# Performance work log

Hardware: AMD Instinct MI355X
Metric: run time of the kernel (lower is better)

Reference implementation:

```python
import jax, jax.numpy as jnp
import numpy as np

N = 100000      # nodes
E = 1600000     # edges (avg degree 16)
D_IN = 256
D_OUT = 128

def setup_inputs() -> dict:
    key = jax.random.key(0)
    k1, k2, k3, k4, k5 = jax.random.split(key, 5)
    x = jax.random.normal(k1, (N, D_IN), dtype=jnp.float32)
    row = jax.random.randint(k2, (E,), 0, N)           # destination node of each edge (adj row index)
    col = jax.random.randint(k3, (E,), 0, N)           # source node (adj col index)
    vals = jnp.ones((E,), dtype=jnp.float32)           # adjacency values
    W = jax.random.normal(k4, (D_IN, D_OUT), dtype=jnp.float32) * (1.0 / np.sqrt(D_IN))
    b = jax.random.normal(k5, (D_OUT,), dtype=jnp.float32) * 0.01
    return {"x": x, "row": row, "col": col, "vals": vals, "W": W, "b": b}

def reference(x, row, col, vals, W, b):
    # support = Linear(x)
    support = x @ W + b                                   # [N, D_OUT]
    # symmetric normalization: D^-1/2 A D^-1/2 (degree = row sums of adj)
    deg = jax.ops.segment_sum(vals, row, num_segments=N)  # [N]
    d_inv_sqrt = jnp.where(deg > 0, jax.lax.rsqrt(jnp.maximum(deg, 1e-12)), 0.0)
    norm_vals = vals * d_inv_sqrt[row] * d_inv_sqrt[col]  # [E]
    # output = spmm(adj_norm, support): gather source features, scale, scatter-add to rows
    out = jax.ops.segment_sum(norm_vals[:, None] * support[col], row, num_segments=N)  # [N, D_OUT]
    return out
```

## Files before the change

kernel.cpp:

```cpp
#include <hip/hip_runtime.h>
#include <hip/hip_bf16.h>

#define DIN 256
#define DOUT 128

typedef float f32x4 __attribute__((ext_vector_type(4)));
typedef __bf16 bf16x8 __attribute__((ext_vector_type(8)));
typedef unsigned short u16x8 __attribute__((ext_vector_type(8)));

__device__ __forceinline__ unsigned short f2bf(float f) {
    __bf16 h = (__bf16)f;
    return *(unsigned short*)&h;
}

__global__ void gcn_zero(int* __restrict__ cnt, int N) {
    int i = blockIdx.x * blockDim.x + threadIdx.x;
    if (i < N) cnt[i] = 0;
}

__global__ void gcn_count(const int* __restrict__ row, int* __restrict__ cnt,
                          int* __restrict__ rank, int E) {
    int e = blockIdx.x * blockDim.x + threadIdx.x;
    if (e < E) {
        int r = row[e];
        rank[e] = atomicAdd(&cnt[r], 1);
    }
}

__global__ void gcn_scan_partial(const int* __restrict__ cnt, int* __restrict__ blk, int N) {
    int b = blockIdx.x, t = threadIdx.x;
    int base = b * 1024 + t * 4;
    int s = 0;
#pragma unroll
    for (int k = 0; k < 4; ++k) { int i = base + k; if (i < N) s += cnt[i]; }
    for (int d = 32; d >= 1; d >>= 1) s += __shfl_down(s, d, 64);
    __shared__ int wsum[4];
    int lane = t & 63, wid = t >> 6;
    if (lane == 0) wsum[wid] = s;
    __syncthreads();
    if (t == 0) blk[b] = wsum[0] + wsum[1] + wsum[2] + wsum[3];
}

__global__ void gcn_scan_blk(int* __restrict__ blk, int nblk) {
    if (threadIdx.x == 0) {
        int run = 0;
        for (int i = 0; i < nblk; ++i) { int v = blk[i]; blk[i] = run; run += v; }
    }
}

__global__ void gcn_scan_final(const int* __restrict__ cnt, const int* __restrict__ blk,
                               int* __restrict__ row_ptr, int N, int E) {
    int b = blockIdx.x, t = threadIdx.x;
    int base = b * 1024 + t * 4;
    int v[4]; int s = 0;
#pragma unroll
    for (int k = 0; k < 4; ++k) { int i = base + k; v[k] = (i < N) ? cnt[i] : 0; s += v[k]; }
    int mysum = s;
    int lane = t & 63, wid = t >> 6;
    for (int d = 1; d < 64; d <<= 1) {
        int tt = __shfl_up(s, d, 64);
        if (lane >= d) s += tt;
    }
    __shared__ int wsum[4];
    if (lane == 63) wsum[wid] = s;
    __syncthreads();
    int woff = 0;
    for (int w = 0; w < wid; ++w) woff += wsum[w];
    int excl = blk[b] + woff + (s - mysum);
#pragma unroll
    for (int k = 0; k < 4; ++k) {
        int i = base + k;
        if (i < N) row_ptr[i] = excl;
        excl += v[k];
    }
    if (b == (int)gridDim.x - 1 && t == (int)blockDim.x - 1) row_ptr[N] = E;
}

__global__ void gcn_fill(const int* __restrict__ row, const int* __restrict__ col,
                         const float* __restrict__ vals, const int* __restrict__ row_ptr,
                         const int* __restrict__ rank, int2* __restrict__ csr, int E) {
    int e = blockIdx.x * blockDim.x + threadIdx.x;
    if (e < E) {
        int r = row[e];
        int p = row_ptr[r] + rank[e];
        int2 pk;
        pk.x = col[e];
        pk.y = __float_as_int(vals[e]);
        csr[p] = pk;
    }
}

__global__ void gcn_degdinv(const int* __restrict__ row_ptr, const int2* __restrict__ csr,
                            float* __restrict__ dinv, int N) {
    int r = blockIdx.x * blockDim.x + threadIdx.x;
    if (r < N) {
        int b = row_ptr[r], e = row_ptr[r + 1];
        float s = 0.f;
        for (int j = b; j < e; ++j) s += __int_as_float(csr[j].y);
        dinv[r] = (s > 0.f) ? rsqrtf(fmaxf(s, 1e-12f)) : 0.f;
    }
}

__global__ void gcn_norm(const int* __restrict__ row_ptr, const float* __restrict__ dinv,
                         int2* __restrict__ csr, int N) {
    int r = blockIdx.x * blockDim.x + threadIdx.x;
    if (r < N) {
        int b = row_ptr[r], e = row_ptr[r + 1];
        float dr = dinv[r];
        for (int j = b; j < e; ++j) {
            int2 p = csr[j];
            csr[j].y = __float_as_int(__int_as_float(p.y) * dr * dinv[p.x]);
        }
    }
}

__global__ void gcn_wconv(const float* __restrict__ W, unsigned short* __restrict__ Wt) {
    int id = blockIdx.x * blockDim.x + threadIdx.x;
    int c = id >> 8;
    int k = id & 255;
    Wt[c * 256 + k] = f2bf(W[k * DOUT + c]);
}

__global__ __launch_bounds__(256) void gcn_gemm(const float* __restrict__ x,
                                                const unsigned short* __restrict__ Wt,
                                                const float* __restrict__ bias,
                                                unsigned short* __restrict__ support, int N) {
    __shared__ unsigned short xs[128][72];
    __shared__ unsigned short wl[128][72];

    int t = threadIdx.x;
    int n0 = blockIdx.x * 128;
    int l = t & 63;
    int w = t >> 6;
    int w32 = w * 32;
    int lr = l & 15;
    int lk = (l >> 4) * 8;

    f32x4 acc[2][8] = {};

    int srow = t >> 1;
    int skk = (t & 1) * 32;

    for (int kt = 0; kt < DIN; kt += 64) {
        {
            float4 f[8];
            if (n0 + srow < N) {
                const float4* src = (const float4*)&x[(size_t)(n0 + srow) * DIN + kt + skk];
#pragma unroll
                for (int i = 0; i < 8; ++i) f[i] = src[i];
            } else {
#pragma unroll
                for (int i = 0; i < 8; ++i) f[i] = make_float4(0, 0, 0, 0);
            }
#pragma unroll
            for (int i = 0; i < 4; ++i) {
                u16x8 pk;
                pk[0] = f2bf(f[2 * i].x);     pk[1] = f2bf(f[2 * i].y);
                pk[2] = f2bf(f[2 * i].z);     pk[3] = f2bf(f[2 * i].w);
                pk[4] = f2bf(f[2 * i + 1].x); pk[5] = f2bf(f[2 * i + 1].y);
                pk[6] = f2bf(f[2 * i + 1].z); pk[7] = f2bf(f[2 * i + 1].w);
                *(u16x8*)&xs[srow][skk + 8 * i] = pk;
            }
        }
        {
            const u16x8* src = (const u16x8*)&Wt[(size_t)srow * DIN + kt + skk];
#pragma unroll
            for (int i = 0; i < 4; ++i) *(u16x8*)&wl[srow][skk + 8 * i] = src[i];
        }
        __syncthreads();
#pragma unroll
        for (int ks = 0; ks < 2; ++ks) {
            bf16x8 a[2], b[8];
#pragma unroll
            for (int m = 0; m < 2; ++m)
                a[m] = *(const bf16x8*)&xs[w32 + m * 16 + lr][ks * 32 + lk];
#pragma unroll
            for (int n = 0; n < 8; ++n)
                b[n] = *(const bf16x8*)&wl[n * 16 + lr][ks * 32 + lk];
#pragma unroll
            for (int m = 0; m < 2; ++m)
#pragma unroll
                for (int n = 0; n < 8; ++n)
                    acc[m][n] = __builtin_amdgcn_mfma_f32_16x16x32_bf16(a[m], b[n], acc[m][n], 0, 0, 0);
        }
        __syncthreads();
    }

    float bias_v[8];
#pragma unroll
    for (int n = 0; n < 8; ++n) bias_v[n] = bias[n * 16 + lr];

    int rbase = n0 + w32 + (l >> 4) * 4;
#pragma unroll
    for (int m = 0; m < 2; ++m) {
#pragma unroll
        for (int r = 0; r < 4; ++r) {
            int rowi = rbase + m * 16 + r;
            if (rowi < N) {
                unsigned short* dst = &support[(size_t)rowi * DOUT + lr];
#pragma unroll
                for (int n = 0; n < 8; ++n)
                    dst[n * 16] = f2bf(acc[m][n][r] + bias_v[n]);
            }
        }
    }
}

__global__ __launch_bounds__(256) void gcn_spmm(const int* __restrict__ row_ptr,
                                                const int2* __restrict__ csr,
                                                const unsigned short* __restrict__ support,
                                                float* __restrict__ out, int N) {
    int wid = threadIdx.x >> 6;
    int lane = threadIdx.x & 63;
    int r = blockIdx.x * 4 + wid;
    if (r >= N) return;
    int beg = row_ptr[r], end = row_ptr[r + 1];
    float accx = 0.f, accy = 0.f;

    for (int base = beg; base < end; base += 64) {
        int nj = end - base; if (nj > 64) nj = 64;
        int2 e = make_int2(0, 0);
        if (base + lane < end) e = csr[base + lane];
        for (int j = 0; j < nj; ++j) {
            int c = __shfl(e.x, j, 64);
            float v = __int_as_float(__shfl(e.y, j, 64));
            unsigned int p = *(const unsigned int*)&support[(size_t)c * DOUT + lane * 2];
            accx += v * __uint_as_float(p << 16);
            accy += v * __uint_as_float(p & 0xffff0000u);
        }
    }
    float2 o; o.x = accx; o.y = accy;
    *(float2*)&out[(size_t)r * DOUT + lane * 2] = o;
}

extern "C" void kernel_launch(void* const* d_in, const int* in_sizes, int n_in,
                              void* d_out, int out_size, void* d_ws, size_t ws_size,
                              hipStream_t stream) {
    const float* x    = (const float*)d_in[0];
    const int*   row  = (const int*)d_in[1];
    const int*   col  = (const int*)d_in[2];
    const float* vals = (const float*)d_in[3];
    const float* W    = (const float*)d_in[4];
    const float* bias = (const float*)d_in[5];
    float* out = (float*)d_out;

    int N = in_sizes[0] / DIN;
    int E = in_sizes[1];
    int NBLK = (N + 1023) / 1024;

    char* ws = (char*)d_ws;
    size_t off = 0;
    auto take = [&](size_t bytes) -> char* {
        char* p = ws + off;
        off = (off + bytes + 255) & ~(size_t)255;
        return p;
    };
    float* dinv    = (float*)take((size_t)N * 4);
    int*   cnt     = (int*)take((size_t)N * 4);
    int*   row_ptr = (int*)take((size_t)(N + 1) * 4);
    int*   blk     = (int*)take((size_t)NBLK * 4);
    int*   rank    = (int*)take((size_t)E * 4);
    int2*  csr     = (int2*)take((size_t)E * 8);
    unsigned short* Wt      = (unsigned short*)take((size_t)DIN * DOUT * 2);
    unsigned short* support = (unsigned short*)take((size_t)N * DOUT * 2);
    (void)ws_size;

    int nbN = (N + 255) / 256;
    int nbE = (E + 255) / 256;

    gcn_zero<<<nbN, 256, 0, stream>>>(cnt, N);
    gcn_count<<<nbE, 256, 0, stream>>>(row, cnt, rank, E);
    gcn_scan_partial<<<NBLK, 256, 0, stream>>>(cnt, blk, N);
    gcn_scan_blk<<<1, 64, 0, stream>>>(blk, NBLK);
    gcn_scan_final<<<NBLK, 256, 0, stream>>>(cnt, blk, row_ptr, N, E);
    gcn_fill<<<nbE, 256, 0, stream>>>(row, col, vals, row_ptr, rank, csr, E);
    gcn_degdinv<<<nbN, 256, 0, stream>>>(row_ptr, csr, dinv, N);
    gcn_norm<<<nbN, 256, 0, stream>>>(row_ptr, dinv, csr, N);
    gcn_wconv<<<(DIN * DOUT) / 256, 256, 0, stream>>>(W, Wt);
    gcn_gemm<<<(N + 127) / 128, 256, 0, stream>>>(x, Wt, bias, support, N);
    gcn_spmm<<<(N + 3) / 4, 256, 0, stream>>>(row_ptr, csr, support, out, N);
}
```

Before: 453.2 us.

## Fuse edge counting into GEMM launch and widen per-row parallelism in sparse kernels

Extra blocks are appended to the GEMM grid so edge counting with atomics runs concurrently with the dense GEMM, and a memset replaces the zero kernel. The degree and normalization kernels now use 16 lanes per row instead of one thread per row, so edge data is read coalesced. SpMM splits each wavefront into four groups that handle four edges at once with 16-byte loads of eight bf16 features, then reduces across groups with shuffles. This targets launch overhead, uncoalesced per-row loops, and narrow gathers. The cost is extra shuffle reductions and possible imbalance between GEMM and atomic blocks.

```diff
diff --git a/kernel.cpp b/kernel.cpp
--- a/kernel.cpp
+++ b/kernel.cpp
@@ -13,17 +13,102 @@
     return *(unsigned short*)&h;
 }
 
-__global__ void gcn_zero(int* __restrict__ cnt, int N) {
-    int i = blockIdx.x * blockDim.x + threadIdx.x;
-    if (i < N) cnt[i] = 0;
-}
-
-__global__ void gcn_count(const int* __restrict__ row, int* __restrict__ cnt,
-                          int* __restrict__ rank, int E) {
-    int e = blockIdx.x * blockDim.x + threadIdx.x;
-    if (e < E) {
-        int r = row[e];
-        rank[e] = atomicAdd(&cnt[r], 1);
+__global__ void gcn_wconv(const float* __restrict__ W, unsigned short* __restrict__ Wt) {
+    int id = blockIdx.x * blockDim.x + threadIdx.x;
+    int c = id >> 8;
+    int k = id & 255;
+    Wt[c * 256 + k] = f2bf(W[k * DOUT + c]);
+}
+
+__global__ __launch_bounds__(256) void gcn_gemm_count(
+        const float* __restrict__ x, const unsigned short* __restrict__ Wt,
+        const float* __restrict__ bias, unsigned short* __restrict__ support,
+        const int* __restrict__ row, int* __restrict__ cnt, int* __restrict__ rank,
+        int N, int E, int nbG) {
+    __shared__ unsigned short xs[128][72];
+    __shared__ unsigned short wl[128][72];
+
+    if ((int)blockIdx.x >= nbG) {
+        int e = ((int)blockIdx.x - nbG) * 256 + threadIdx.x;
+        if (e < E) rank[e] = atomicAdd(&cnt[row[e]], 1);
+        return;
+    }
+
+    int t = threadIdx.x;
+    int n0 = blockIdx.x * 128;
+    int l = t & 63;
+    int w = t >> 6;
+    int w32 = w * 32;
+    int lr = l & 15;
+    int lk = (l >> 4) * 8;
+
+    f32x4 acc[2][8] = {};
+
+    int srow = t >> 1;
+    int skk = (t & 1) * 32;
+
+    for (int kt = 0; kt < DIN; kt += 64) {
+        {
+            float4 f[8];
+            if (n0 + srow < N) {
+                const float4* src = (const float4*)&x[(size_t)(n0 + srow) * DIN + kt + skk];
+#pragma unroll
+                for (int i = 0; i < 8; ++i) f[i] = src[i];
+            } else {
+#pragma unroll
+                for (int i = 0; i < 8; ++i) f[i] = make_float4(0, 0, 0, 0);
+            }
+#pragma unroll
+            for (int i = 0; i < 4; ++i) {
+                u16x8 pk;
+                pk[0] = f2bf(f[2 * i].x);     pk[1] = f2bf(f[2 * i].y);
+                pk[2] = f2bf(f[2 * i].z);     pk[3] = f2bf(f[2 * i].w);
+                pk[4] = f2bf(f[2 * i + 1].x); pk[5] = f2bf(f[2 * i + 1].y);
+                pk[6] = f2bf(f[2 * i + 1].z); pk[7] = f2bf(f[2 * i + 1].w);
+                *(u16x8*)&xs[srow][skk + 8 * i] = pk;
+            }
+        }
+        {
+            const u16x8* src = (const u16x8*)&Wt[(size_t)srow * DIN + kt + skk];
+#pragma unroll
+            for (int i = 0; i < 4; ++i) *(u16x8*)&wl[srow][skk + 8 * i] = src[i];
+        }
+        __syncthreads();
+#pragma unroll
+        for (int ks = 0; ks < 2; ++ks) {
+            bf16x8 a[2], b[8];
+#pragma unroll
+            for (int m = 0; m < 2; ++m)
+                a[m] = *(const bf16x8*)&xs[w32 + m * 16 + lr][ks * 32 + lk];
+#pragma unroll
+            for (int n = 0; n < 8; ++n)
+                b[n] = *(const bf16x8*)&wl[n * 16 + lr][ks * 32 + lk];
+#pragma unroll
+            for (int m = 0; m < 2; ++m)
+#pragma unroll
+                for (int n = 0; n < 8; ++n)
+                    acc[m][n] = __builtin_amdgcn_mfma_f32_16x16x32_bf16(a[m], b[n], acc[m][n], 0, 0, 0);
+        }
+        __syncthreads();
+    }
+
+    float bias_v[8];
+#pragma unroll
+    for (int n = 0; n < 8; ++n) bias_v[n] = bias[n * 16 + lr];
+
+    int rbase = n0 + w32 + (l >> 4) * 4;
+#pragma unroll
+    for (int m = 0; m < 2; ++m) {
+#pragma unroll
+        for (int r = 0; r < 4; ++r) {
+            int rowi = rbase + m * 16 + r;
+            if (rowi < N) {
+                unsigned short* dst = &support[(size_t)rowi * DOUT + lr];
+#pragma unroll
+                for (int n = 0; n < 8; ++n)
+                    dst[n * 16] = f2bf(acc[m][n][r] + bias_v[n]);
+            }
+        }
     }
 }
 
@@ -90,119 +175,35 @@
     }
 }
 
-__global__ void gcn_degdinv(const int* __restrict__ row_ptr, const int2* __restrict__ csr,
-                            float* __restrict__ dinv, int N) {
-    int r = blockIdx.x * blockDim.x + threadIdx.x;
-    if (r < N) {
-        int b = row_ptr[r], e = row_ptr[r + 1];
-        float s = 0.f;
-        for (int j = b; j < e; ++j) s += __int_as_float(csr[j].y);
-        dinv[r] = (s > 0.f) ? rsqrtf(fmaxf(s, 1e-12f)) : 0.f;
-    }
-}
-
-__global__ void gcn_norm(const int* __restrict__ row_ptr, const float* __restrict__ dinv,
-                         int2* __restrict__ csr, int N) {
-    int r = blockIdx.x * blockDim.x + threadIdx.x;
-    if (r < N) {
-        int b = row_ptr[r], e = row_ptr[r + 1];
-        float dr = dinv[r];
-        for (int j = b; j < e; ++j) {
-            int2 p = csr[j];
-            csr[j].y = __float_as_int(__int_as_float(p.y) * dr * dinv[p.x]);
-        }
-    }
-}
-
-__global__ void gcn_wconv(const float* __restrict__ W, unsigned short* __restrict__ Wt) {
-    int id = blockIdx.x * blockDim.x + threadIdx.x;
-    int c = id >> 8;
-    int k = id & 255;
-    Wt[c * 256 + k] = f2bf(W[k * DOUT + c]);
-}
-
-__global__ __launch_bounds__(256) void gcn_gemm(const float* __restrict__ x,
-                                                const unsigned short* __restrict__ Wt,
-                                                const float* __restrict__ bias,
-                                                unsigned short* __restrict__ support, int N) {
-    __shared__ unsigned short xs[128][72];
-    __shared__ unsigned short wl[128][72];
-
+__global__ __launch_bounds__(256) void gcn_degdinv(const int* __restrict__ row_ptr,
+                                                   const int2* __restrict__ csr,
+                                                   float* __restrict__ dinv, int N) {
     int t = threadIdx.x;
-    int n0 = blockIdx.x * 128;
-    int l = t & 63;
-    int w = t >> 6;
-    int w32 = w * 32;
-    int lr = l & 15;
-    int lk = (l >> 4) * 8;
-
-    f32x4 acc[2][8] = {};
-
-    int srow = t >> 1;
-    int skk = (t & 1) * 32;
-
-    for (int kt = 0; kt < DIN; kt += 64) {
-        {
-            float4 f[8];
-            if (n0 + srow < N) {
-                const float4* src = (const float4*)&x[(size_t)(n0 + srow) * DIN + kt + skk];
-#pragma unroll
-                for (int i = 0; i < 8; ++i) f[i] = src[i];
-            } else {
-#pragma unroll
-                for (int i = 0; i < 8; ++i) f[i] = make_float4(0, 0, 0, 0);
-            }
-#pragma unroll
-            for (int i = 0; i < 4; ++i) {
-                u16x8 pk;
-                pk[0] = f2bf(f[2 * i].x);     pk[1] = f2bf(f[2 * i].y);
-                pk[2] = f2bf(f[2 * i].z);     pk[3] = f2bf(f[2 * i].w);
-                pk[4] = f2bf(f[2 * i + 1].x); pk[5] = f2bf(f[2 * i + 1].y);
-                pk[6] = f2bf(f[2 * i + 1].z); pk[7] = f2bf(f[2 * i + 1].w);
-                *(u16x8*)&xs[srow][skk + 8 * i] = pk;
-            }
-        }
-        {
-            const u16x8* src = (const u16x8*)&Wt[(size_t)srow * DIN + kt + skk];
-#pragma unroll
-            for (int i = 0; i < 4; ++i) *(u16x8*)&wl[srow][skk + 8 * i] = src[i];
-        }
-        __syncthreads();
-#pragma unroll
-        for (int ks = 0; ks < 2; ++ks) {
-            bf16x8 a[2], b[8];
-#pragma unroll
-            for (int m = 0; m < 2; ++m)
-                a[m] = *(const bf16x8*)&xs[w32 + m * 16 + lr][ks * 32 + lk];
-#pragma unroll
-            for (int n = 0; n < 8; ++n)
-                b[n] = *(const bf16x8*)&wl[n * 16 + lr][ks * 32 + lk];
-#pragma unroll
-            for (int m = 0; m < 2; ++m)
-#pragma unroll
-                for (int n = 0; n < 8; ++n)
-                    acc[m][n] = __builtin_amdgcn_mfma_f32_16x16x32_bf16(a[m], b[n], acc[m][n], 0, 0, 0);
-        }
-        __syncthreads();
-    }
-
-    float bias_v[8];
-#pragma unroll
-    for (int n = 0; n < 8; ++n) bias_v[n] = bias[n * 16 + lr];
-
-    int rbase = n0 + w32 + (l >> 4) * 4;
-#pragma unroll
-    for (int m = 0; m < 2; ++m) {
-#pragma unroll
-        for (int r = 0; r < 4; ++r) {
-            int rowi = rbase + m * 16 + r;
-            if (rowi < N) {
-                unsigned short* dst = &support[(size_t)rowi * DOUT + lr];
-#pragma unroll
-                for (int n = 0; n < 8; ++n)
-                    dst[n * 16] = f2bf(acc[m][n][r] + bias_v[n]);
-            }
-        }
+    int fl = t & 15;
+    int r = blockIdx.x * 16 + (t >> 4);
+    if (r >= N) return;
+    int beg = row_ptr[r], end = row_ptr[r + 1];
+    float s = 0.f;
+    for (int j = beg + fl; j < end; j += 16) s += __int_as_float(csr[j].y);
+    s += __shfl_xor(s, 1, 64);
+    s += __shfl_xor(s, 2, 64);
+    s += __shfl_xor(s, 4, 64);
+    s += __shfl_xor(s, 8, 64);
+    if (fl == 0) dinv[r] = (s > 0.f) ? rsqrtf(fmaxf(s, 1e-12f)) : 0.f;
+}
+
+__global__ __launch_bounds__(256) void gcn_norm(const int* __restrict__ row_ptr,
+                                                const float* __restrict__ dinv,
+                                                int2* __restrict__ csr, int N) {
+    int t = threadIdx.x;
+    int fl = t & 15;
+    int r = blockIdx.x * 16 + (t >> 4);
+    if (r >= N) return;
+    int beg = row_ptr[r], end = row_ptr[r + 1];
+    float dr = dinv[r];
+    for (int j = beg + fl; j < end; j += 16) {
+        int2 p = csr[j];
+        csr[j].y = __float_as_int(__int_as_float(p.y) * dr * dinv[p.x]);
     }
 }
 
@@ -215,22 +216,45 @@
     int r = blockIdx.x * 4 + wid;
     if (r >= N) return;
     int beg = row_ptr[r], end = row_ptr[r + 1];
-    float accx = 0.f, accy = 0.f;
+    int g = lane >> 4;
+    int fl = lane & 15;
+    float acc[8] = {};
 
     for (int base = beg; base < end; base += 64) {
         int nj = end - base; if (nj > 64) nj = 64;
         int2 e = make_int2(0, 0);
         if (base + lane < end) e = csr[base + lane];
-        for (int j = 0; j < nj; ++j) {
-            int c = __shfl(e.x, j, 64);
-            float v = __int_as_float(__shfl(e.y, j, 64));
-            unsigned int p = *(const unsigned int*)&support[(size_t)c * DOUT + lane * 2];
-            accx += v * __uint_as_float(p << 16);
-            accy += v * __uint_as_float(p & 0xffff0000u);
-        }
-    }
-    float2 o; o.x = accx; o.y = accy;
-    *(float2*)&out[(size_t)r * DOUT + lane * 2] = o;
+        int nchunk = (nj + 3) >> 2;
+        for (int q = 0; q < nchunk; ++q) {
+            int idx = q * 4 + g;
+            int c = __shfl(e.x, idx, 64);
+            float v = __int_as_float(__shfl(e.y, idx, 64));
+            if (idx < nj) {
+                uint4 p = *(const uint4*)&support[(size_t)c * DOUT + fl * 8];
+                acc[0] += v * __uint_as_float(p.x << 16);
+                acc[1] += v * __uint_as_float(p.x & 0xffff0000u);
+                acc[2] += v * __uint_as_float(p.y << 16);
+                acc[3] += v * __uint_as_float(p.y & 0xffff0000u);
+                acc[4] += v * __uint_as_float(p.z << 16);
+                acc[5] += v * __uint_as_float(p.z & 0xffff0000u);
+                acc[6] += v * __uint_as_float(p.w << 16);
+                acc[7] += v * __uint_as_float(p.w & 0xffff0000u);
+            }
+        }
+    }
+#pragma unroll
+    for (int i = 0; i < 8; ++i) {
+        acc[i] += __shfl_xor(acc[i], 16, 64);
+        acc[i] += __shfl_xor(acc[i], 32, 64);
+    }
+    if (g == 0) {
+        float4 o0, o1;
+        o0.x = acc[0]; o0.y = acc[1]; o0.z = acc[2]; o0.w = acc[3];
+        o1.x = acc[4]; o1.y = acc[5]; o1.z = acc[6]; o1.w = acc[7];
+        float* dst = &out[(size_t)r * DOUT + fl * 8];
+        *(float4*)dst = o0;
+        *(float4*)(dst + 4) = o1;
+    }
 }
 
 extern "C" void kernel_launch(void* const* d_in, const int* in_sizes, int n_in,
@@ -265,18 +289,17 @@
     unsigned short* support = (unsigned short*)take((size_t)N * DOUT * 2);
     (void)ws_size;
 
-    int nbN = (N + 255) / 256;
     int nbE = (E + 255) / 256;
-
-    gcn_zero<<<nbN, 256, 0, stream>>>(cnt, N);
-    gcn_count<<<nbE, 256, 0, stream>>>(row, cnt, rank, E);
+    int nbG = (N + 127) / 128;
+
+    hipMemsetAsync(cnt, 0, (size_t)N * 4, stream);
+    gcn_wconv<<<(DIN * DOUT) / 256, 256, 0, stream>>>(W, Wt);
+    gcn_gemm_count<<<nbG + nbE, 256, 0, stream>>>(x, Wt, bias, support, row, cnt, rank, N, E, nbG);
     gcn_scan_partial<<<NBLK, 256, 0, stream>>>(cnt, blk, N);
     gcn_scan_blk<<<1, 64, 0, stream>>>(blk, NBLK);
     gcn_scan_final<<<NBLK, 256, 0, stream>>>(cnt, blk, row_ptr, N, E);
     gcn_fill<<<nbE, 256, 0, stream>>>(row, col, vals, row_ptr, rank, csr, E);
-    gcn_degdinv<<<nbN, 256, 0, stream>>>(row_ptr, csr, dinv, N);
-    gcn_norm<<<nbN, 256, 0, stream>>>(row_ptr, dinv, csr, N);
-    gcn_wconv<<<(DIN * DOUT) / 256, 256, 0, stream>>>(W, Wt);
-    gcn_gemm<<<(N + 127) / 128, 256, 0, stream>>>(x, Wt, bias, support, N);
+    gcn_degdinv<<<(N + 15) / 16, 256, 0, stream>>>(row_ptr, csr, dinv, N);
+    gcn_norm<<<(N + 15) / 16, 256, 0, stream>>>(row_ptr, dinv, csr, N);
     gcn_spmm<<<(N + 3) / 4, 256, 0, stream>>>(row_ptr, csr, support, out, N);
 }
```

Measured after the change: 390.0 us. 1.16x faster.
